# Kernel tuning notes

Measured on AMD Instinct MI355X. Metric: run time of the kernel, lower is better.

The kernel has to match this reference:

```python
import jax, jax.numpy as jnp
from jax import lax
import numpy as np


def conv4d(x, w, b, pad):
    """4D conv (stride 1) as a sum of 3D convs over the first-spatial-dim kernel taps.
    x: [B, Cin, T, D, H, W]; w: [Cout, Cin, Kt, Kd, Kh, Kw]; same pad on all dims."""
    B, Cin, T, D, H, W = x.shape
    Cout, _, Kt = w.shape[:3]
    xp = jnp.pad(x, ((0, 0), (0, 0), (pad, pad), (0, 0), (0, 0), (0, 0)))
    Tout = T + 2 * pad - Kt + 1
    acc = None
    for k in range(Kt):  # loop over kernel taps (<=3), not data dims
        xs = xp[:, :, k:k + Tout]                      # [B,Cin,Tout,D,H,W]
        xs = xs.transpose(0, 2, 1, 3, 4, 5).reshape(B * Tout, Cin, D, H, W)
        y = lax.conv_general_dilated(
            xs, w[:, :, k], (1, 1, 1), [(pad, pad)] * 3,
            dimension_numbers=('NCDHW', 'OIDHW', 'NCDHW'))
        acc = y if acc is None else acc + y
    Do, Ho, Wo = acc.shape[2:]
    out = acc.reshape(B, Tout, Cout, Do, Ho, Wo).transpose(0, 2, 1, 3, 4, 5)
    return out + b[None, :, None, None, None, None]


def tconv4d_k2s2(x, w, b):
    """4D transposed conv, kernel=2, stride=2, pad=0 (non-overlapping blocks).
    x: [B,Cin,T,D,H,W]; w: [Cin,Cout,2,2,2,2] (PyTorch ConvTranspose layout)."""
    B, Cin, T, D, H, W = x.shape
    Cout = w.shape[1]
    y = jnp.einsum('bcijkl,copqrs->boipjqkrls', x, w)
    y = y.reshape(B, Cout, 2 * T, 2 * D, 2 * H, 2 * W)
    return y + b[None, :, None, None, None, None]


def setup_inputs() -> dict:
    key = jax.random.key(0)
    ks = jax.random.split(key, 10)
    Cin, Cout = 64, 32
    x1 = jax.random.normal(ks[0], (2, Cin, 8, 8, 8, 8), dtype=jnp.float32)
    x2 = jax.random.normal(ks[1], (2, Cin // 2, 16, 16, 16, 16), dtype=jnp.float32)
    def w(k, shape, fan_in):
        return jax.random.normal(k, shape, dtype=jnp.float32) / np.float32(np.sqrt(fan_in))
    up_w = w(ks[2], (Cin, Cin // 2, 2, 2, 2, 2), Cin * 16)
    up_b = w(ks[3], (Cin // 2,), Cin * 16)
    w1 = w(ks[4], (Cout, Cin, 3, 3, 3, 3), Cin * 81)
    b1 = w(ks[5], (Cout,), Cin * 81)
    w2 = w(ks[6], (Cout, Cout, 3, 3, 3, 3), Cout * 81)
    b2 = w(ks[7], (Cout,), Cout * 81)
    w3 = w(ks[8], (Cout, Cin, 1, 1, 1, 1), Cin)
    b3 = w(ks[9], (Cout,), Cin)
    return {'x1': x1, 'x2': x2, 'up_w': up_w, 'up_b': up_b,
            'w1': w1, 'b1': b1, 'w2': w2, 'b2': b2, 'w3': w3, 'b3': b3}


def reference(x1, x2, up_w, up_b, w1, b1, w2, b2, w3, b3):
    x1u = tconv4d_k2s2(x1, up_w, up_b)              # [B, Cin//2, 16,16,16,16]
    xc = jnp.concatenate([x2, x1u], axis=1)          # [B, Cin, 16,16,16,16]
    Y = jax.nn.relu(conv4d(xc, w1, b1, 1))
    Y = conv4d(Y, w2, b2, 1)
    sc = conv4d(xc, w3, b3, 0)                       # 1x1 residual projection
    return jax.nn.relu(Y + sc)
```

## Files before the change

### kernel.cpp

```cpp
#include <hip/hip_runtime.h>

typedef unsigned short u16;
typedef __attribute__((ext_vector_type(8))) short short8;
typedef __attribute__((ext_vector_type(4))) float f32x4;

#define XCB_OFF  0
#define Y1B_OFF  8388608
#define W1P_OFF  12582912
#define W2P_OFF  12748800
#define W3P_OFF  12831744
#define UPWP_OFF 12833792
#define X1T_OFF  12866560

__device__ __forceinline__ u16 f2bf(float v) {
    unsigned u = __builtin_bit_cast(unsigned, v);
    u += 0x7FFFu + ((u >> 16) & 1u);
    return (u16)(u >> 16);
}

__device__ __forceinline__ f32x4 MFMA(short8 a, short8 b, f32x4 c) {
    return __builtin_amdgcn_mfma_f32_16x16x32_bf16(a, b, c, 0, 0, 0);
}

__device__ __forceinline__ void decode_bid(int bid, int& b, int& t, int& d, int& h0) {
    int xcd = bid & 7, loc = bid >> 3;
    int hB = loc & 1;
    d = (loc >> 1) & 15;
    int tsub = (loc >> 5) & 1;
    b = loc >> 6;
    t = xcd * 2 + tsub;
    h0 = hB * 8;
}

__global__ __launch_bounds__(256) void setup(const float* __restrict__ w1,
                                             const float* __restrict__ w2,
                                             const float* __restrict__ w3,
                                             const float* __restrict__ upw,
                                             const float* __restrict__ x1,
                                             const float* __restrict__ x2,
                                             u16* __restrict__ ws) {
    __shared__ u16 lds[256 * 66];
    int bid = blockIdx.x;
    int tid = threadIdx.x;
    if (bid < 1108) {
        int idx = bid * 256 + tid;
        if (idx < 165888) {
            int j = idx & 7, lane = (idx >> 3) & 63, rest = idx >> 9;
            int half = rest & 1, chunk = (rest >> 1) & 1, tap = rest >> 2;
            int co = half * 16 + (lane & 15), ci = chunk * 32 + (lane >> 4) * 8 + j;
            ws[W1P_OFF + idx] = f2bf(w1[(co * 64 + ci) * 81 + tap]);
        } else if (idx < 165888 + 82944) {
            int i2 = idx - 165888;
            int j = i2 & 7, lane = (i2 >> 3) & 63, rest = i2 >> 9;
            int half = rest & 1, tap = rest >> 1;
            int co = half * 16 + (lane & 15), ci = (lane >> 4) * 8 + j;
            ws[W2P_OFF + i2] = f2bf(w2[(co * 32 + ci) * 81 + tap]);
        } else if (idx < 165888 + 82944 + 2048) {
            int i3 = idx - (165888 + 82944);
            int j = i3 & 7, lane = (i3 >> 3) & 63, rest = i3 >> 9;
            int half = rest & 1, chunk = rest >> 1;
            int co = half * 16 + (lane & 15), ci = chunk * 32 + (lane >> 4) * 8 + j;
            ws[W3P_OFF + i3] = f2bf(w3[co * 64 + ci]);
        } else if (idx < 250880 + 32768) {
            int i4 = idx - 250880;
            int j = i4 & 7, lane = (i4 >> 3) & 63, rest = i4 >> 9;
            int half = rest & 1, chunk = (rest >> 1) & 1, tap = rest >> 2;
            int co = half * 16 + (lane & 15), ci = chunk * 32 + (lane >> 4) * 8 + j;
            ws[UPWP_OFF + i4] = f2bf(upw[(ci * 32 + co) * 16 + tap]);
        }
    } else if (bid < 1620) {
        int lb = bid - 1108;
        int b = lb >> 8;
        int pos_base = (lb & 255) * 256;
        u16* xcb = ws + XCB_OFF;
        #pragma unroll
        for (int c = 0; c < 32; ++c) {
            lds[tid * 40 + c] = f2bf(x2[((b * 32 + c) << 16) + pos_base + tid]);
        }
        __syncthreads();
        #pragma unroll
        for (int k = 0; k < 4; ++k) {
            int f = k * 256 + tid;
            int u = f & 3, pos = f >> 2;
            uint4 v = *(const uint4*)(lds + pos * 40 + u * 8);
            *(uint4*)(xcb + (size_t)((b << 16) + pos_base + pos) * 64 + u * 8) = v;
        }
    } else {
        int lb = bid - 1620;
        int b = lb >> 4;
        int pos_base = (lb & 15) * 256;
        u16* x1t = ws + X1T_OFF;
        #pragma unroll
        for (int c = 0; c < 64; ++c) {
            lds[tid * 66 + c] = f2bf(x1[((b * 64 + c) << 12) + pos_base + tid]);
        }
        __syncthreads();
        #pragma unroll
        for (int k = 0; k < 64; ++k) {
            int f = k * 256 + tid;
            int ci = f & 63, pos = f >> 6;
            x1t[(size_t)((b << 12) + pos_base + pos) * 64 + ci] = lds[pos * 66 + ci];
        }
    }
}

__global__ __launch_bounds__(256) void xc_up_mfma(const u16* __restrict__ x1t,
                                                  const u16* __restrict__ upwp,
                                                  const float* __restrict__ up_b,
                                                  u16* __restrict__ xcb) {
    int tid = threadIdx.x;
    int wv = tid >> 6, lane = tid & 63;
    int q = lane >> 4, m = lane & 15;
    int wid = blockIdx.x * 4 + wv;
    int j = wid & 63, tap = (wid >> 6) & 15, b = wid >> 10;

    f32x4 acc[4][2];
    {
        float4 bi0 = ((const float4*)up_b)[q];
        float4 bi1 = ((const float4*)up_b)[4 + q];
        #pragma unroll
        for (int g = 0; g < 4; ++g) {
            acc[g][0] = (f32x4){bi0.x, bi0.y, bi0.z, bi0.w};
            acc[g][1] = (f32x4){bi1.x, bi1.y, bi1.z, bi1.w};
        }
    }

    const short8* wv8 = (const short8*)upwp;
    const u16* xb = x1t + (size_t)((b << 12) + (j << 6) + m) * 64;
    #pragma unroll
    for (int chunk = 0; chunk < 2; ++chunk) {
        short8 a0 = wv8[((tap * 2 + chunk) * 2 + 0) * 64 + lane];
        short8 a1 = wv8[((tap * 2 + chunk) * 2 + 1) * 64 + lane];
        #pragma unroll
        for (int g = 0; g < 4; ++g) {
            short8 bf = *(const short8*)(xb + (size_t)(g * 16) * 64 + chunk * 32 + q * 8);
            acc[g][0] = MFMA(a0, bf, acc[g][0]);
            acc[g][1] = MFMA(a1, bf, acc[g][1]);
        }
    }

    int it = j >> 3, id = j & 7;
    int pt = tap >> 3, pd = (tap >> 2) & 1, ph = (tap >> 1) & 1, pw = tap & 1;
    int oT = 2 * it + pt, oD = 2 * id + pd, oW = 2 * (m & 7) + pw;
    #pragma unroll
    for (int g = 0; g < 4; ++g) {
        int ih = g * 2 + (m >> 3);
        int opos = oT * 4096 + oD * 256 + (2 * ih + ph) * 16 + oW;
        u16* op = xcb + (size_t)((b << 16) + opos) * 64 + 32 + q * 4;
        #pragma unroll
        for (int half = 0; half < 2; ++half) {
            f32x4 v = acc[g][half];
            uint2 o;
            o.x = (unsigned)f2bf(v.x) | ((unsigned)f2bf(v.y) << 16);
            o.y = (unsigned)f2bf(v.z) | ((unsigned)f2bf(v.w) << 16);
            *(uint2*)(op + half * 16) = o;
        }
    }
}

__global__ __launch_bounds__(256, 4) void conv1_mfma(const u16* __restrict__ xcb,
                                                     const u16* __restrict__ w1p,
                                                     const float* __restrict__ b1,
                                                     u16* __restrict__ y1b) {
    __shared__ u16 lds[11520];
    int tid = threadIdx.x;
    int lane = tid & 63, wv = tid >> 6;
    int q = lane >> 4, m = lane & 15;
    int c = wv & 1, rg = wv >> 1;
    int b, t, d, h0;
    decode_bid(blockIdx.x, b, t, d, h0);

    int lofs[6], gofs[6];
    bool st[6], inr[6];
    #pragma unroll
    for (int k = 0; k < 6; ++k) {
        int ui = tid + k * 256;
        int u = ui & 7, p = (ui >> 3) % 18, hh = ui / 144;
        int gh = h0 - 1 + hh, gw = p - 1;
        st[k] = ui < 1440;
        inr[k] = st[k] && ((unsigned)gh < 16u) && ((unsigned)gw < 16u);
        gofs[k] = (gh * 16 + gw) * 64 + u * 8;
        lofs[k] = hh * 1152 + p * 64 + ((u ^ (p & 7)) * 8);
    }

    f32x4 acc[4][2];
    if (c == 0) {
        float4 bi0 = ((const float4*)b1)[q];
        float4 bi1 = ((const float4*)b1)[4 + q];
        #pragma unroll
        for (int i = 0; i < 4; ++i) {
            acc[i][0] = (f32x4){bi0.x, bi0.y, bi0.z, bi0.w};
            acc[i][1] = (f32x4){bi1.x, bi1.y, bi1.z, bi1.w};
        }
    } else {
        #pragma unroll
        for (int i = 0; i < 4; ++i) {
            acc[i][0] = (f32x4){0.f, 0.f, 0.f, 0.f};
            acc[i][1] = (f32x4){0.f, 0.f, 0.f, 0.f};
        }
    }
    const short8* w1v = (const short8*)w1p;

    uint4 rP[6];
    auto load_plane = [&](int ktd) {
        int kt = ktd / 3, kd = ktd - kt * 3;
        int tt = t + kt - 1, dd = d + kd - 1;
        bool pv = ((unsigned)tt < 16u) && ((unsigned)dd < 16u);
        const u16* src = xcb + (size_t)(size_t)(((b * 16 + tt) * 16 + dd)) * 16384;
        #pragma unroll
        for (int k = 0; k < 6; ++k) {
            uint4 v = {0, 0, 0, 0};
            if (pv && inr[k]) v = *(const uint4*)(src + gofs[k]);
            rP[k] = v;
        }
    };
    auto write_plane = [&]() {
        #pragma unroll
        for (int k = 0; k < 6; ++k)
            if (st[k]) *(uint4*)(lds + lofs[k]) = rP[k];
    };

    load_plane(0);
    for (int ktd = 0; ktd < 9; ++ktd) {
        __syncthreads();
        write_plane();
        if (ktd < 8) load_plane(ktd + 1);
        __syncthreads();
        #pragma unroll
        for (int kw = 0; kw < 3; ++kw) {
            int p = kw + m, pm = p & 7;
            int bo = p * 64 + ((((c << 2) | q) ^ pm) << 3);
            short8 R[6];
            #pragma unroll
            for (int r = 0; r < 6; ++r)
                R[r] = *(const short8*)(lds + (rg * 4 + r) * 1152 + bo);
            #pragma unroll
            for (int kh = 0; kh < 3; ++kh) {
                int tap = (ktd * 3 + kh) * 3 + kw;
                short8 a0 = w1v[((tap * 2 + c) * 2 + 0) * 64 + lane];
                short8 a1 = w1v[((tap * 2 + c) * 2 + 1) * 64 + lane];
                #pragma unroll
                for (int i = 0; i < 4; ++i) {
                    acc[i][0] = MFMA(a0, R[i + kh], acc[i][0]);
                    acc[i][1] = MFMA(a1, R[i + kh], acc[i][1]);
                }
            }
        }
    }

    __syncthreads();
    f32x4* buf = (f32x4*)lds;
    if (c == 1) {
        #pragma unroll
        for (int i = 0; i < 4; ++i)
            #pragma unroll
            for (int half = 0; half < 2; ++half)
                buf[((rg * 4 + i) * 2 + half) * 64 + lane] = acc[i][half];
    }
    __syncthreads();
    if (c == 0) {
        int obase = ((b * 16 + t) * 16 + d) * 256 + (h0 + rg * 4) * 16 + m;
        #pragma unroll
        for (int i = 0; i < 4; ++i) {
            int pos = obase + i * 16;
            #pragma unroll
            for (int half = 0; half < 2; ++half) {
                f32x4 v = acc[i][half];
                f32x4 w = buf[((rg * 4 + i) * 2 + half) * 64 + lane];
                v.x += w.x; v.y += w.y; v.z += w.z; v.w += w.w;
                unsigned r0 = f2bf(fmaxf(v.x, 0.f)), r1 = f2bf(fmaxf(v.y, 0.f));
                unsigned r2 = f2bf(fmaxf(v.z, 0.f)), r3 = f2bf(fmaxf(v.w, 0.f));
                uint2 o;
                o.x = r0 | (r1 << 16);
                o.y = r2 | (r3 << 16);
                *(uint2*)(y1b + (size_t)pos * 32 + half * 16 + q * 4) = o;
            }
        }
    }
}

__global__ __launch_bounds__(256, 4) void conv2_mfma(const u16* __restrict__ y1b,
                                                     const u16* __restrict__ xcb,
                                                     const u16* __restrict__ w2p,
                                                     const u16* __restrict__ w3p,
                                                     const float* __restrict__ b2,
                                                     const float* __restrict__ b3,
                                                     float* __restrict__ out) {
    __shared__ u16 lds[5760];
    int tid = threadIdx.x;
    int lane = tid & 63, wv = tid >> 6;
    int q = lane >> 4, m = lane & 15;
    int hf = wv & 1, rg = wv >> 1;
    int b, t, d, h0;
    decode_bid(blockIdx.x, b, t, d, h0);

    int lofs[3], gofs[3];
    bool st[3], inr[3];
    #pragma unroll
    for (int k = 0; k < 3; ++k) {
        int ui = tid + k * 256;
        int u = ui & 3, p = (ui >> 2) % 18, hh = ui / 72;
        int gh = h0 - 1 + hh, gw = p - 1;
        st[k] = ui < 720;
        inr[k] = st[k] && ((unsigned)gh < 16u) && ((unsigned)gw < 16u);
        gofs[k] = (gh * 16 + gw) * 32 + u * 8;
        lofs[k] = hh * 576 + p * 32 + ((u ^ (p & 3)) * 8);
    }

    f32x4 acc[4];
    {
        float4 p0 = ((const float4*)b2)[hf * 4 + q];
        float4 s0 = ((const float4*)b3)[hf * 4 + q];
        #pragma unroll
        for (int i = 0; i < 4; ++i)
            acc[i] = (f32x4){p0.x + s0.x, p0.y + s0.y, p0.z + s0.z, p0.w + s0.w};
    }
    const short8* w2v = (const short8*)w2p;

    uint4 rP[3];
    auto load_plane = [&](int ktd) {
        int kt = ktd / 3, kd = ktd - kt * 3;
        int tt = t + kt - 1, dd = d + kd - 1;
        bool pv = ((unsigned)tt < 16u) && ((unsigned)dd < 16u);
        const u16* src = y1b + (size_t)(size_t)(((b * 16 + tt) * 16 + dd)) * 8192;
        #pragma unroll
        for (int k = 0; k < 3; ++k) {
            uint4 v = {0, 0, 0, 0};
            if (pv && inr[k]) v = *(const uint4*)(src + gofs[k]);
            rP[k] = v;
        }
    };
    auto write_plane = [&]() {
        #pragma unroll
        for (int k = 0; k < 3; ++k)
            if (st[k]) *(uint4*)(lds + lofs[k]) = rP[k];
    };

    load_plane(0);
    for (int ktd = 0; ktd < 9; ++ktd) {
        __syncthreads();
        write_plane();
        if (ktd < 8) load_plane(ktd + 1);
        __syncthreads();
        #pragma unroll
        for (int kw = 0; kw < 3; ++kw) {
            int p = kw + m, pm = p & 3;
            int bo = p * 32 + ((q ^ pm) << 3);
            short8 R[6];
            #pragma unroll
            for (int r = 0; r < 6; ++r)
                R[r] = *(const short8*)(lds + (rg * 4 + r) * 576 + bo);
            #pragma unroll
            for (int kh = 0; kh < 3; ++kh) {
                int tap = (ktd * 3 + kh) * 3 + kw;
                short8 a = w2v[(tap * 2 + hf) * 64 + lane];
                #pragma unroll
                for (int i = 0; i < 4; ++i) {
                    acc[i] = MFMA(a, R[i + kh], acc[i]);
                }
            }
        }
    }

    const short8* w3v = (const short8*)w3p;
    int lpos0 = (t * 16 + d) * 256 + (h0 + rg * 4) * 16 + m;
    int gpos0 = (b << 16) + lpos0;
    #pragma unroll
    for (int chunk = 0; chunk < 2; ++chunk) {
        short8 a = w3v[(chunk * 2 + hf) * 64 + lane];
        #pragma unroll
        for (int i = 0; i < 4; ++i) {
            short8 bf = *(const short8*)(xcb + (size_t)(gpos0 + i * 16) * 64 + ((chunk << 2) | q) * 8);
            acc[i] = MFMA(a, bf, acc[i]);
        }
    }

    #pragma unroll
    for (int i = 0; i < 4; ++i) {
        int lpos = lpos0 + i * 16;
        f32x4 v = acc[i];
        int co = hf * 16 + q * 4;
        float* op = out + (((size_t)(b * 32 + co)) << 16) + lpos;
        op[0ull << 16] = fmaxf(v.x, 0.f);
        op[1ull << 16] = fmaxf(v.y, 0.f);
        op[2ull << 16] = fmaxf(v.z, 0.f);
        op[3ull << 16] = fmaxf(v.w, 0.f);
    }
}

extern "C" void kernel_launch(void* const* d_in, const int* in_sizes, int n_in,
                              void* d_out, int out_size, void* d_ws, size_t ws_size,
                              hipStream_t stream) {
    const float* x1   = (const float*)d_in[0];
    const float* x2   = (const float*)d_in[1];
    const float* up_w = (const float*)d_in[2];
    const float* up_b = (const float*)d_in[3];
    const float* w1   = (const float*)d_in[4];
    const float* b1   = (const float*)d_in[5];
    const float* w2   = (const float*)d_in[6];
    const float* b2   = (const float*)d_in[7];
    const float* w3   = (const float*)d_in[8];
    const float* b3   = (const float*)d_in[9];
    u16* ws  = (u16*)d_ws;
    float* out = (float*)d_out;

    setup<<<1652, 256, 0, stream>>>(w1, w2, w3, up_w, x1, x2, ws);
    xc_up_mfma<<<512, 256, 0, stream>>>(ws + X1T_OFF, ws + UPWP_OFF, up_b, ws + XCB_OFF);
    conv1_mfma<<<1024, 256, 0, stream>>>(ws + XCB_OFF, ws + W1P_OFF, b1, ws + Y1B_OFF);
    conv2_mfma<<<1024, 256, 0, stream>>>(ws + Y1B_OFF, ws + XCB_OFF, ws + W2P_OFF,
                                         ws + W3P_OFF, b2, b3, out);
}
```

Measured before the change: 169.3 us.

## Fuse upsample into setup, widen conv blocks, skip padded planes

The separate upsample kernel is folded into the setup kernel. Upsample blocks now read fp32 x1 directly, convert it on the fly, and stage the per-tap transposed-conv weights in LDS, which removes the x1t/upwp workspace passes and one launch. Both 3x3x3x3 conv kernels move to 512-thread blocks where each wave computes two output rows instead of four, which lowers per-wave register and MFMA load. Plane lists now drop out-of-range t/d taps instead of loading zeros and doing MFMAs on them, and each block starts at a rotated plane so concurrent blocks hit different memory. The costs are strided fp32 gathers in the upsample path and more halo rereads from LDS per output row.

```diff
diff --git a/kernel.cpp b/kernel.cpp
--- a/kernel.cpp
+++ b/kernel.cpp
@@ -9,8 +9,6 @@
 #define W1P_OFF  12582912
 #define W2P_OFF  12748800
 #define W3P_OFF  12831744
-#define UPWP_OFF 12833792
-#define X1T_OFF  12866560
 
 __device__ __forceinline__ u16 f2bf(float v) {
     unsigned u = __builtin_bit_cast(unsigned, v);
@@ -32,17 +30,18 @@
     h0 = hB * 8;
 }
 
-__global__ __launch_bounds__(256) void setup(const float* __restrict__ w1,
-                                             const float* __restrict__ w2,
-                                             const float* __restrict__ w3,
-                                             const float* __restrict__ upw,
-                                             const float* __restrict__ x1,
-                                             const float* __restrict__ x2,
-                                             u16* __restrict__ ws) {
-    __shared__ u16 lds[256 * 66];
+__global__ __launch_bounds__(256) void stage1(const float* __restrict__ w1,
+                                              const float* __restrict__ w2,
+                                              const float* __restrict__ w3,
+                                              const float* __restrict__ upw,
+                                              const float* __restrict__ up_b,
+                                              const float* __restrict__ x1,
+                                              const float* __restrict__ x2,
+                                              u16* __restrict__ ws) {
+    __shared__ u16 lds[10240];
     int bid = blockIdx.x;
     int tid = threadIdx.x;
-    if (bid < 1108) {
+    if (bid < 980) {
         int idx = bid * 256 + tid;
         if (idx < 165888) {
             int j = idx & 7, lane = (idx >> 3) & 63, rest = idx >> 9;
@@ -55,21 +54,15 @@
             int half = rest & 1, tap = rest >> 1;
             int co = half * 16 + (lane & 15), ci = (lane >> 4) * 8 + j;
             ws[W2P_OFF + i2] = f2bf(w2[(co * 32 + ci) * 81 + tap]);
-        } else if (idx < 165888 + 82944 + 2048) {
+        } else {
             int i3 = idx - (165888 + 82944);
             int j = i3 & 7, lane = (i3 >> 3) & 63, rest = i3 >> 9;
             int half = rest & 1, chunk = rest >> 1;
             int co = half * 16 + (lane & 15), ci = chunk * 32 + (lane >> 4) * 8 + j;
             ws[W3P_OFF + i3] = f2bf(w3[co * 64 + ci]);
-        } else if (idx < 250880 + 32768) {
-            int i4 = idx - 250880;
-            int j = i4 & 7, lane = (i4 >> 3) & 63, rest = i4 >> 9;
-            int half = rest & 1, chunk = (rest >> 1) & 1, tap = rest >> 2;
-            int co = half * 16 + (lane & 15), ci = chunk * 32 + (lane >> 4) * 8 + j;
-            ws[UPWP_OFF + i4] = f2bf(upw[(ci * 32 + co) * 16 + tap]);
-        }
-    } else if (bid < 1620) {
-        int lb = bid - 1108;
+        }
+    } else if (bid < 1492) {
+        int lb = bid - 980;
         int b = lb >> 8;
         int pos_base = (lb & 255) * 256;
         u16* xcb = ws + XCB_OFF;
@@ -86,79 +79,74 @@
             *(uint4*)(xcb + (size_t)((b << 16) + pos_base + pos) * 64 + u * 8) = v;
         }
     } else {
-        int lb = bid - 1620;
-        int b = lb >> 4;
-        int pos_base = (lb & 15) * 256;
-        u16* x1t = ws + X1T_OFF;
-        #pragma unroll
-        for (int c = 0; c < 64; ++c) {
-            lds[tid * 66 + c] = f2bf(x1[((b * 64 + c) << 12) + pos_base + tid]);
-        }
-        __syncthreads();
-        #pragma unroll
-        for (int k = 0; k < 64; ++k) {
-            int f = k * 256 + tid;
-            int ci = f & 63, pos = f >> 6;
-            x1t[(size_t)((b << 12) + pos_base + pos) * 64 + ci] = lds[pos * 66 + ci];
-        }
-    }
-}
-
-__global__ __launch_bounds__(256) void xc_up_mfma(const u16* __restrict__ x1t,
-                                                  const u16* __restrict__ upwp,
-                                                  const float* __restrict__ up_b,
-                                                  u16* __restrict__ xcb) {
-    int tid = threadIdx.x;
-    int wv = tid >> 6, lane = tid & 63;
-    int q = lane >> 4, m = lane & 15;
-    int wid = blockIdx.x * 4 + wv;
-    int j = wid & 63, tap = (wid >> 6) & 15, b = wid >> 10;
-
-    f32x4 acc[4][2];
-    {
-        float4 bi0 = ((const float4*)up_b)[q];
-        float4 bi1 = ((const float4*)up_b)[4 + q];
+        int lb = bid - 1492;
+        int wv = tid >> 6, lane = tid & 63;
+        int q = lane >> 4, m = lane & 15;
+        int wid = lb * 4 + wv;
+        int j = wid & 63, tap = (wid >> 6) & 15, b = wid >> 10;
+
+        {
+            int chunk = tid >> 7, half = (tid >> 6) & 1, l2 = tid & 63;
+            int co = half * 16 + (l2 & 15), qq = (l2 >> 4) & 3;
+            #pragma unroll
+            for (int jj = 0; jj < 8; ++jj) {
+                int ci = chunk * 32 + qq * 8 + jj;
+                lds[(((chunk * 2 + half) * 64) + l2) * 8 + jj] =
+                    f2bf(upw[(ci * 32 + co) * 16 + tap]);
+            }
+        }
+        __syncthreads();
+
+        f32x4 acc[4][2];
+        {
+            float4 bi0 = ((const float4*)up_b)[q];
+            float4 bi1 = ((const float4*)up_b)[4 + q];
+            #pragma unroll
+            for (int g = 0; g < 4; ++g) {
+                acc[g][0] = (f32x4){bi0.x, bi0.y, bi0.z, bi0.w};
+                acc[g][1] = (f32x4){bi1.x, bi1.y, bi1.z, bi1.w};
+            }
+        }
+        const float* xb = x1 + (size_t)(b * 64) * 4096;
+        int ipos0 = j * 64 + m;
+        #pragma unroll
+        for (int chunk = 0; chunk < 2; ++chunk) {
+            short8 a0 = *(const short8*)(lds + ((chunk * 2 + 0) * 64 + lane) * 8);
+            short8 a1 = *(const short8*)(lds + ((chunk * 2 + 1) * 64 + lane) * 8);
+            #pragma unroll
+            for (int g = 0; g < 4; ++g) {
+                short8 bf;
+                #pragma unroll
+                for (int jj = 0; jj < 8; ++jj) {
+                    int ci = chunk * 32 + q * 8 + jj;
+                    bf[jj] = (short)f2bf(xb[(size_t)ci * 4096 + ipos0 + g * 16]);
+                }
+                acc[g][0] = MFMA(a0, bf, acc[g][0]);
+                acc[g][1] = MFMA(a1, bf, acc[g][1]);
+            }
+        }
+        u16* xcb = ws + XCB_OFF;
+        int it = j >> 3, id = j & 7;
+        int pt = tap >> 3, pd = (tap >> 2) & 1, ph = (tap >> 1) & 1, pw = tap & 1;
+        int oT = 2 * it + pt, oD = 2 * id + pd, oW = 2 * (m & 7) + pw;
         #pragma unroll
         for (int g = 0; g < 4; ++g) {
-            acc[g][0] = (f32x4){bi0.x, bi0.y, bi0.z, bi0.w};
-            acc[g][1] = (f32x4){bi1.x, bi1.y, bi1.z, bi1.w};
-        }
-    }
-
-    const short8* wv8 = (const short8*)upwp;
-    const u16* xb = x1t + (size_t)((b << 12) + (j << 6) + m) * 64;
-    #pragma unroll
-    for (int chunk = 0; chunk < 2; ++chunk) {
-        short8 a0 = wv8[((tap * 2 + chunk) * 2 + 0) * 64 + lane];
-        short8 a1 = wv8[((tap * 2 + chunk) * 2 + 1) * 64 + lane];
-        #pragma unroll
-        for (int g = 0; g < 4; ++g) {
-            short8 bf = *(const short8*)(xb + (size_t)(g * 16) * 64 + chunk * 32 + q * 8);
-            acc[g][0] = MFMA(a0, bf, acc[g][0]);
-            acc[g][1] = MFMA(a1, bf, acc[g][1]);
-        }
-    }
-
-    int it = j >> 3, id = j & 7;
-    int pt = tap >> 3, pd = (tap >> 2) & 1, ph = (tap >> 1) & 1, pw = tap & 1;
-    int oT = 2 * it + pt, oD = 2 * id + pd, oW = 2 * (m & 7) + pw;
-    #pragma unroll
-    for (int g = 0; g < 4; ++g) {
-        int ih = g * 2 + (m >> 3);
-        int opos = oT * 4096 + oD * 256 + (2 * ih + ph) * 16 + oW;
-        u16* op = xcb + (size_t)((b << 16) + opos) * 64 + 32 + q * 4;
-        #pragma unroll
-        for (int half = 0; half < 2; ++half) {
-            f32x4 v = acc[g][half];
-            uint2 o;
-            o.x = (unsigned)f2bf(v.x) | ((unsigned)f2bf(v.y) << 16);
-            o.y = (unsigned)f2bf(v.z) | ((unsigned)f2bf(v.w) << 16);
-            *(uint2*)(op + half * 16) = o;
-        }
-    }
-}
-
-__global__ __launch_bounds__(256, 4) void conv1_mfma(const u16* __restrict__ xcb,
+            int ih = g * 2 + (m >> 3);
+            int opos = oT * 4096 + oD * 256 + (2 * ih + ph) * 16 + oW;
+            u16* op = xcb + (size_t)((b << 16) + opos) * 64 + 32 + q * 4;
+            #pragma unroll
+            for (int half = 0; half < 2; ++half) {
+                f32x4 v = acc[g][half];
+                uint2 o;
+                o.x = (unsigned)f2bf(v.x) | ((unsigned)f2bf(v.y) << 16);
+                o.y = (unsigned)f2bf(v.z) | ((unsigned)f2bf(v.w) << 16);
+                *(uint2*)(op + half * 16) = o;
+            }
+        }
+    }
+}
+
+__global__ __launch_bounds__(512, 8) void conv1_mfma(const u16* __restrict__ xcb,
                                                      const u16* __restrict__ w1p,
                                                      const float* __restrict__ b1,
                                                      u16* __restrict__ y1b) {
@@ -170,11 +158,11 @@
     int b, t, d, h0;
     decode_bid(blockIdx.x, b, t, d, h0);
 
-    int lofs[6], gofs[6];
-    bool st[6], inr[6];
-    #pragma unroll
-    for (int k = 0; k < 6; ++k) {
-        int ui = tid + k * 256;
+    int lofs[3], gofs[3];
+    bool st[3], inr[3];
+    #pragma unroll
+    for (int k = 0; k < 3; ++k) {
+        int ui = tid + k * 512;
         int u = ui & 7, p = (ui >> 3) % 18, hh = ui / 144;
         int gh = h0 - 1 + hh, gw = p - 1;
         st[k] = ui < 1440;
@@ -183,64 +171,77 @@
         lofs[k] = hh * 1152 + p * 64 + ((u ^ (p & 7)) * 8);
     }
 
-    f32x4 acc[4][2];
+    f32x4 acc[2][2];
     if (c == 0) {
         float4 bi0 = ((const float4*)b1)[q];
         float4 bi1 = ((const float4*)b1)[4 + q];
         #pragma unroll
-        for (int i = 0; i < 4; ++i) {
+        for (int i = 0; i < 2; ++i) {
             acc[i][0] = (f32x4){bi0.x, bi0.y, bi0.z, bi0.w};
             acc[i][1] = (f32x4){bi1.x, bi1.y, bi1.z, bi1.w};
         }
     } else {
         #pragma unroll
-        for (int i = 0; i < 4; ++i) {
+        for (int i = 0; i < 2; ++i) {
             acc[i][0] = (f32x4){0.f, 0.f, 0.f, 0.f};
             acc[i][1] = (f32x4){0.f, 0.f, 0.f, 0.f};
         }
     }
     const short8* w1v = (const short8*)w1p;
 
-    uint4 rP[6];
-    auto load_plane = [&](int ktd) {
+    int pl[9], np = 0;
+    #pragma unroll
+    for (int ktd = 0; ktd < 9; ++ktd) {
         int kt = ktd / 3, kd = ktd - kt * 3;
         int tt = t + kt - 1, dd = d + kd - 1;
-        bool pv = ((unsigned)tt < 16u) && ((unsigned)dd < 16u);
-        const u16* src = xcb + (size_t)(size_t)(((b * 16 + tt) * 16 + dd)) * 16384;
-        #pragma unroll
-        for (int k = 0; k < 6; ++k) {
+        if (((unsigned)tt < 16u) && ((unsigned)dd < 16u))
+            pl[np++] = (ktd << 16) | ((b * 16 + tt) * 16 + dd);
+    }
+    int rot = (blockIdx.x * 5) % np;
+
+    uint4 rP[3];
+    auto load_plane = [&](int pidx) {
+        const u16* src = xcb + (size_t)pidx * 16384;
+        #pragma unroll
+        for (int k = 0; k < 3; ++k) {
             uint4 v = {0, 0, 0, 0};
-            if (pv && inr[k]) v = *(const uint4*)(src + gofs[k]);
+            if (inr[k]) v = *(const uint4*)(src + gofs[k]);
             rP[k] = v;
         }
     };
     auto write_plane = [&]() {
         #pragma unroll
-        for (int k = 0; k < 6; ++k)
+        for (int k = 0; k < 3; ++k)
             if (st[k]) *(uint4*)(lds + lofs[k]) = rP[k];
     };
 
-    load_plane(0);
-    for (int ktd = 0; ktd < 9; ++ktd) {
+    load_plane(pl[rot] & 0xffff);
+    for (int s = 0; s < np; ++s) {
+        int idx = rot + s; if (idx >= np) idx -= np;
+        int cur = pl[idx];
         __syncthreads();
         write_plane();
-        if (ktd < 8) load_plane(ktd + 1);
-        __syncthreads();
+        if (s + 1 < np) {
+            int nx = rot + s + 1; if (nx >= np) nx -= np;
+            load_plane(pl[nx] & 0xffff);
+        }
+        __syncthreads();
+        int ktd = cur >> 16;
         #pragma unroll
         for (int kw = 0; kw < 3; ++kw) {
             int p = kw + m, pm = p & 7;
             int bo = p * 64 + ((((c << 2) | q) ^ pm) << 3);
-            short8 R[6];
-            #pragma unroll
-            for (int r = 0; r < 6; ++r)
-                R[r] = *(const short8*)(lds + (rg * 4 + r) * 1152 + bo);
+            short8 R[4];
+            #pragma unroll
+            for (int r = 0; r < 4; ++r)
+                R[r] = *(const short8*)(lds + (rg * 2 + r) * 1152 + bo);
             #pragma unroll
             for (int kh = 0; kh < 3; ++kh) {
                 int tap = (ktd * 3 + kh) * 3 + kw;
                 short8 a0 = w1v[((tap * 2 + c) * 2 + 0) * 64 + lane];
                 short8 a1 = w1v[((tap * 2 + c) * 2 + 1) * 64 + lane];
                 #pragma unroll
-                for (int i = 0; i < 4; ++i) {
+                for (int i = 0; i < 2; ++i) {
                     acc[i][0] = MFMA(a0, R[i + kh], acc[i][0]);
                     acc[i][1] = MFMA(a1, R[i + kh], acc[i][1]);
                 }
@@ -252,21 +253,21 @@
     f32x4* buf = (f32x4*)lds;
     if (c == 1) {
         #pragma unroll
-        for (int i = 0; i < 4; ++i)
+        for (int i = 0; i < 2; ++i)
             #pragma unroll
             for (int half = 0; half < 2; ++half)
-                buf[((rg * 4 + i) * 2 + half) * 64 + lane] = acc[i][half];
+                buf[((rg * 2 + i) * 2 + half) * 64 + lane] = acc[i][half];
     }
     __syncthreads();
     if (c == 0) {
-        int obase = ((b * 16 + t) * 16 + d) * 256 + (h0 + rg * 4) * 16 + m;
-        #pragma unroll
-        for (int i = 0; i < 4; ++i) {
+        int obase = ((b * 16 + t) * 16 + d) * 256 + (h0 + rg * 2) * 16 + m;
+        #pragma unroll
+        for (int i = 0; i < 2; ++i) {
             int pos = obase + i * 16;
             #pragma unroll
             for (int half = 0; half < 2; ++half) {
                 f32x4 v = acc[i][half];
-                f32x4 w = buf[((rg * 4 + i) * 2 + half) * 64 + lane];
+                f32x4 w = buf[((rg * 2 + i) * 2 + half) * 64 + lane];
                 v.x += w.x; v.y += w.y; v.z += w.z; v.w += w.w;
                 unsigned r0 = f2bf(fmaxf(v.x, 0.f)), r1 = f2bf(fmaxf(v.y, 0.f));
                 unsigned r2 = f2bf(fmaxf(v.z, 0.f)), r3 = f2bf(fmaxf(v.w, 0.f));
@@ -279,7 +280,7 @@
     }
 }
 
-__global__ __launch_bounds__(256, 4) void conv2_mfma(const u16* __restrict__ y1b,
+__global__ __launch_bounds__(512, 8) void conv2_mfma(const u16* __restrict__ y1b,
                                                      const u16* __restrict__ xcb,
                                                      const u16* __restrict__ w2p,
                                                      const u16* __restrict__ w3p,
@@ -294,11 +295,11 @@
     int b, t, d, h0;
     decode_bid(blockIdx.x, b, t, d, h0);
 
-    int lofs[3], gofs[3];
-    bool st[3], inr[3];
-    #pragma unroll
-    for (int k = 0; k < 3; ++k) {
-        int ui = tid + k * 256;
+    int lofs[2], gofs[2];
+    bool st[2], inr[2];
+    #pragma unroll
+    for (int k = 0; k < 2; ++k) {
+        int ui = tid + k * 512;
         int u = ui & 3, p = (ui >> 2) % 18, hh = ui / 72;
         int gh = h0 - 1 + hh, gw = p - 1;
         st[k] = ui < 720;
@@ -307,55 +308,68 @@
         lofs[k] = hh * 576 + p * 32 + ((u ^ (p & 3)) * 8);
     }
 
-    f32x4 acc[4];
+    f32x4 acc[2];
     {
         float4 p0 = ((const float4*)b2)[hf * 4 + q];
         float4 s0 = ((const float4*)b3)[hf * 4 + q];
         #pragma unroll
-        for (int i = 0; i < 4; ++i)
+        for (int i = 0; i < 2; ++i)
             acc[i] = (f32x4){p0.x + s0.x, p0.y + s0.y, p0.z + s0.z, p0.w + s0.w};
     }
     const short8* w2v = (const short8*)w2p;
 
-    uint4 rP[3];
-    auto load_plane = [&](int ktd) {
+    int pl[9], np = 0;
+    #pragma unroll
+    for (int ktd = 0; ktd < 9; ++ktd) {
         int kt = ktd / 3, kd = ktd - kt * 3;
         int tt = t + kt - 1, dd = d + kd - 1;
-        bool pv = ((unsigned)tt < 16u) && ((unsigned)dd < 16u);
-        const u16* src = y1b + (size_t)(size_t)(((b * 16 + tt) * 16 + dd)) * 8192;
-        #pragma unroll
-        for (int k = 0; k < 3; ++k) {
+        if (((unsigned)tt < 16u) && ((unsigned)dd < 16u))
+            pl[np++] = (ktd << 16) | ((b * 16 + tt) * 16 + dd);
+    }
+    int rot = (blockIdx.x * 5) % np;
+
+    uint4 rP[2];
+    auto load_plane = [&](int pidx) {
+        const u16* src = y1b + (size_t)pidx * 8192;
+        #pragma unroll
+        for (int k = 0; k < 2; ++k) {
             uint4 v = {0, 0, 0, 0};
-            if (pv && inr[k]) v = *(const uint4*)(src + gofs[k]);
+            if (inr[k]) v = *(const uint4*)(src + gofs[k]);
             rP[k] = v;
         }
     };
     auto write_plane = [&]() {
         #pragma unroll
-        for (int k = 0; k < 3; ++k)
+        for (int k = 0; k < 2; ++k)
             if (st[k]) *(uint4*)(lds + lofs[k]) = rP[k];
     };
 
-    load_plane(0);
-    for (int ktd = 0; ktd < 9; ++ktd) {
+    load_plane(pl[rot] & 0xffff);
+    for (int s = 0; s < np; ++s) {
+        int idx = rot + s; if (idx >= np) idx -= np;
+        int cur = pl[idx];
         __syncthreads();
         write_plane();
-        if (ktd < 8) load_plane(ktd + 1);
-        __syncthreads();
+        if (s + 1 < np) {
+            int nx = rot + s + 1; if (nx >= np) nx -= np;
+            load_plane(pl[nx] & 0xffff);
+        }
+        __syncthreads();
+        int ktd = cur >> 16;
         #pragma unroll
         for (int kw = 0; kw < 3; ++kw) {
             int p = kw + m, pm = p & 3;
             int bo = p * 32 + ((q ^ pm) << 3);
-            short8 R[6];
-            #pragma unroll
-            for (int r = 0; r < 6; ++r)
-                R[r] = *(const short8*)(lds + (rg * 4 + r) * 576 + bo);
+            short8 R[4];
+            #pragma unroll
+            for (int r = 0; r < 4; ++r)
+                R[r] = *(const short8*)(lds + (rg * 2 + r) * 576 + bo);
             #pragma unroll
             for (int kh = 0; kh < 3; ++kh) {
                 int tap = (ktd * 3 + kh) * 3 + kw;
                 short8 a = w2v[(tap * 2 + hf) * 64 + lane];
                 #pragma unroll
-                for (int i = 0; i < 4; ++i) {
+                for (int i = 0; i < 2; ++i) {
                     acc[i] = MFMA(a, R[i + kh], acc[i]);
                 }
             }
@@ -363,20 +377,20 @@
     }
 
     const short8* w3v = (const short8*)w3p;
-    int lpos0 = (t * 16 + d) * 256 + (h0 + rg * 4) * 16 + m;
+    int lpos0 = (t * 16 + d) * 256 + (h0 + rg * 2) * 16 + m;
     int gpos0 = (b << 16) + lpos0;
     #pragma unroll
     for (int chunk = 0; chunk < 2; ++chunk) {
         short8 a = w3v[(chunk * 2 + hf) * 64 + lane];
         #pragma unroll
-        for (int i = 0; i < 4; ++i) {
+        for (int i = 0; i < 2; ++i) {
             short8 bf = *(const short8*)(xcb + (size_t)(gpos0 + i * 16) * 64 + ((chunk << 2) | q) * 8);
             acc[i] = MFMA(a, bf, acc[i]);
         }
     }
 
     #pragma unroll
-    for (int i = 0; i < 4; ++i) {
+    for (int i = 0; i < 2; ++i) {
         int lpos = lpos0 + i * 16;
         f32x4 v = acc[i];
         int co = hf * 16 + q * 4;
@@ -404,9 +418,8 @@
     u16* ws  = (u16*)d_ws;
     float* out = (float*)d_out;
 
-    setup<<<1652, 256, 0, stream>>>(w1, w2, w3, up_w, x1, x2, ws);
-    xc_up_mfma<<<512, 256, 0, stream>>>(ws + X1T_OFF, ws + UPWP_OFF, up_b, ws + XCB_OFF);
-    conv1_mfma<<<1024, 256, 0, stream>>>(ws + XCB_OFF, ws + W1P_OFF, b1, ws + Y1B_OFF);
-    conv2_mfma<<<1024, 256, 0, stream>>>(ws + Y1B_OFF, ws + XCB_OFF, ws + W2P_OFF,
+    stage1<<<2004, 256, 0, stream>>>(w1, w2, w3, up_w, up_b, x1, x2, ws);
+    conv1_mfma<<<1024, 512, 0, stream>>>(ws + XCB_OFF, ws + W1P_OFF, b1, ws + Y1B_OFF);
+    conv2_mfma<<<1024, 512, 0, stream>>>(ws + Y1B_OFF, ws + XCB_OFF, ws + W2P_OFF,
                                          ws + W3P_OFF, b2, b3, out);
 }
```

Measured after the change: 198.4 us. +17.2%, slower.
